# Performance work log

Measured on AMD Instinct MI355X. Metric: run time of the kernel, lower is better.

The kernel has to match this reference:

```python
import jax, jax.numpy as jnp
import numpy as np

B, N, D, NUM_CLASSES = 2048, 32768, 256, 100

def setup_inputs() -> dict:
    key = jax.random.key(0)
    k1, k2, k3 = jax.random.split(key, 3)
    x = jax.random.normal(k1, (B, D), dtype=jnp.float32)
    support_embeddings = jax.random.normal(k2, (N, D), dtype=jnp.float32)
    support_labels = jax.random.randint(k3, (N,), 0, NUM_CLASSES, dtype=jnp.int64)
    return {
        "x": x,
        "support_embeddings": support_embeddings,
        "support_labels": support_labels,
        "num_classes": NUM_CLASSES,
    }

def reference(x, support_embeddings, support_labels, num_classes):
    # Pairwise L2 distance [B, N] via ||q||^2 + ||s||^2 - 2 q.s (avoids [B,N,D] broadcast)
    q2 = jnp.sum(x * x, axis=1, keepdims=True)                 # [B, 1]
    s2 = jnp.sum(support_embeddings * support_embeddings, axis=1)  # [N]
    cross = jnp.einsum('bd,nd->bn', x, support_embeddings)     # [B, N]
    dist = jnp.sqrt(jnp.maximum(q2 + s2[None, :] - 2.0 * cross, 0.0))
    # topk(-dist, k=1) over support axis -> nearest neighbor index
    _, idx = jax.lax.top_k(-dist, 1)                           # [B, 1]
    idx = jnp.squeeze(idx, axis=1)                             # [B]
    labels = jnp.take(support_labels, idx, axis=0)             # [B]
    one_hot = jax.nn.one_hot(labels, num_classes, dtype=jnp.int32)  # [B, num_classes]
    return one_hot
```

## Files before the change

kernel.cpp:

```cpp
#include <hip/hip_runtime.h>

#define BQ 2048
#define NS 32768
#define DIM 256
#define NROWS (NS + BQ)

#define BMQ 128
#define BNS 128
#define BK 32
#define NST (DIM / BK)
#define GY (NS / BNS)
#define GX (BQ / BMQ)
#define EPS 0.08f
#define FBCH GY

typedef _Float16 f16;
typedef _Float16 f16x4 __attribute__((ext_vector_type(4)));
typedef _Float16 f16x8 __attribute__((ext_vector_type(8)));
typedef float    f32x4 __attribute__((ext_vector_type(4)));

__device__ __forceinline__ void gload16(const f16* g, f16* l) {
    __builtin_amdgcn_global_load_lds(
        (const __attribute__((address_space(1))) unsigned int*)g,
        (__attribute__((address_space(3))) unsigned int*)l, 16, 0, 0);
}

__device__ __forceinline__ const f16x8* fragp(const f16* base, int row, int q) {
    return (const f16x8*)(base + row * 32 + ((q ^ ((row >> 1) & 3)) << 3));
}

__global__ __launch_bounds__(256) void convert_kernel(
    const float* __restrict__ x, const float* __restrict__ sup,
    f16* __restrict__ xh, f16* __restrict__ sh,
    float* __restrict__ s2, int* __restrict__ fb_cnt) {
    if (blockIdx.x == 0 && threadIdx.x == 0) *fb_cnt = 0;
    const int wave = threadIdx.x >> 6, lane = threadIdx.x & 63;
    const int row = blockIdx.x * 4 + wave;
    if (row < NS) {
        float4 v = ((const float4*)(sup + (size_t)row * DIM))[lane];
        f16x4 hi;
        hi[0] = (f16)v.x; hi[1] = (f16)v.y; hi[2] = (f16)v.z; hi[3] = (f16)v.w;
        *(f16x4*)(sh + (size_t)row * DIM + lane * 4) = hi;
        float sum = v.x * v.x + v.y * v.y + v.z * v.z + v.w * v.w;
#pragma unroll
        for (int off = 32; off > 0; off >>= 1) sum += __shfl_xor(sum, off);
        if (lane == 0) s2[row] = sum;
    } else {
        const int q = row - NS;
        float4 v = ((const float4*)(x + (size_t)q * DIM))[lane];
        f16x4 hi;
        hi[0] = (f16)v.x; hi[1] = (f16)v.y; hi[2] = (f16)v.z; hi[3] = (f16)v.w;
        *(f16x4*)(xh + (size_t)q * DIM + lane * 4) = hi;
    }
}

__global__ __launch_bounds__(256) void knn_mfma(
    const f16* __restrict__ xh, const f16* __restrict__ sh,
    const float* __restrict__ s2g,
    float* __restrict__ pv1, float* __restrict__ pv2, int* __restrict__ pi1) {
    __shared__ f16 T[3][2][BMQ * 32];

    const int tid  = threadIdx.x;
    const int lane = tid & 63, wid = tid >> 6;
    const int l16  = lane & 15, quad = lane >> 4;

    const int id   = blockIdx.y * GX + blockIdx.x;
    const int xcd  = id & 7;
    const int slot = id >> 3;
    const int gx   = slot & (GX - 1);
    const int gy   = xcd * (GY / 8) + (slot >> 4);
    const int m0   = gx * BMQ;
    const int n0   = gy * BNS;

    const int rl = lane >> 2;
    const int qs = (lane & 3) ^ ((rl >> 1) & 3);
    const size_t srcoff = (size_t)rl * DIM + qs * 8;

    const f16* px0 = xh + (size_t)(m0 + wid * 32) * DIM + srcoff;
    const f16* px1 = px0 + (size_t)16 * DIM;
    const f16* ps0 = sh + (size_t)(n0 + wid * 32) * DIM + srcoff;
    const f16* ps1 = ps0 + (size_t)16 * DIM;
    const int dX = wid * 1024;

    f32x4 acc[2][8];
#pragma unroll
    for (int fi = 0; fi < 2; ++fi)
#pragma unroll
        for (int fj = 0; fj < 8; ++fj) acc[fi][fj] = (f32x4){0.f, 0.f, 0.f, 0.f};

    auto issue = [&](int s) {
        f16* bx = &T[s % 3][0][dX];
        f16* bs = &T[s % 3][1][dX];
        const int k0 = s * BK;
        gload16(px0 + k0, bx);
        gload16(px1 + k0, bx + 512);
        gload16(ps0 + k0, bs);
        gload16(ps1 + k0, bs + 512);
    };

    issue(0);
    issue(1);

#pragma unroll
    for (int s = 0; s < NST; ++s) {
        if (s < NST - 1)
            asm volatile("s_waitcnt vmcnt(4)\n\ts_barrier" ::: "memory");
        else
            asm volatile("s_waitcnt vmcnt(0)\n\ts_barrier" ::: "memory");
        if (s + 2 < NST) issue(s + 2);

        const f16* TX = &T[s % 3][0][0];
        const f16* TS = &T[s % 3][1][0];
        f16x8 A0 = *fragp(TX, wid * 32 + l16,      quad);
        f16x8 A1 = *fragp(TX, wid * 32 + 16 + l16, quad);
#pragma unroll
        for (int fj = 0; fj < 8; ++fj) {
            f16x8 B = *fragp(TS, fj * 16 + l16, quad);
            acc[0][fj] = __builtin_amdgcn_mfma_f32_16x16x32_f16(A0, B, acc[0][fj], 0, 0, 0);
            acc[1][fj] = __builtin_amdgcn_mfma_f32_16x16x32_f16(A1, B, acc[1][fj], 0, 0, 0);
        }
    }

    float s2v[8];
#pragma unroll
    for (int fj = 0; fj < 8; ++fj) s2v[fj] = s2g[n0 + fj * 16 + l16];
#pragma unroll
    for (int fi = 0; fi < 2; ++fi)
#pragma unroll
        for (int rg = 0; rg < 4; ++rg) {
            float bv1 = 3.4e38f, bv2 = 3.4e38f; int bi = 0;
#pragma unroll
            for (int fj = 0; fj < 8; ++fj) {
                float s = fmaf(-2.f, acc[fi][fj][rg], s2v[fj]);
                bv2 = fminf(bv2, fmaxf(bv1, s));
                bi  = (s < bv1) ? (n0 + fj * 16 + l16) : bi;
                bv1 = fminf(bv1, s);
            }
#pragma unroll
            for (int m = 1; m < 16; m <<= 1) {
                float ov1 = __shfl_xor(bv1, m);
                float ov2 = __shfl_xor(bv2, m);
                int   oi  = __shfl_xor(bi, m);
                float nb2 = fminf(fminf(bv2, ov2), fmaxf(bv1, ov1));
                bi  = (ov1 < bv1) ? oi : bi;
                bv1 = fminf(bv1, ov1);
                bv2 = nb2;
            }
            if (l16 == 0) {
                const int row = m0 + wid * 32 + fi * 16 + quad * 4 + rg;
                pv1[(size_t)row * GY + gy] = bv1;
                pv2[(size_t)row * GY + gy] = bv2;
                pi1[(size_t)row * GY + gy] = bi;
            }
        }
}

__global__ __launch_bounds__(128) void finalize2(
    const float* __restrict__ pv1, const float* __restrict__ pv2,
    const int* __restrict__ pi1, const int* __restrict__ labels,
    const int* __restrict__ ncp, int* __restrict__ out,
    int* __restrict__ fb_cnt, int* __restrict__ fb_list,
    float* __restrict__ qbest) {
    const int q = blockIdx.x, tid = threadIdx.x;
    __shared__ int s_label;
    if (tid < 64) {
        float bv1 = 3.4e38f, bv2 = 3.4e38f; int bi = 0;
        for (int t = tid; t < GY; t += 64) {
            float ov1 = pv1[(size_t)q * GY + t];
            float ov2 = pv2[(size_t)q * GY + t];
            int   oi  = pi1[(size_t)q * GY + t];
            float nb2 = fminf(fminf(bv2, ov2), fmaxf(bv1, ov1));
            bi  = (ov1 < bv1) ? oi : bi;
            bv1 = fminf(bv1, ov1);
            bv2 = nb2;
        }
#pragma unroll
        for (int m = 1; m < 64; m <<= 1) {
            float ov1 = __shfl_xor(bv1, m);
            float ov2 = __shfl_xor(bv2, m);
            int   oi  = __shfl_xor(bi, m);
            float nb2 = fminf(fminf(bv2, ov2), fmaxf(bv1, ov1));
            bi  = (ov1 < bv1) ? oi : bi;
            bv1 = fminf(bv1, ov1);
            bv2 = nb2;
        }
        if (tid == 0) {
            qbest[q] = bv1;
            if (bv2 - bv1 <= EPS) {
                int slot = atomicAdd(fb_cnt, 1);
                fb_list[slot] = q;
            }
            bool is64 = true;
            for (int i = 1; i < 128; i += 2)
                if (labels[i] != 0) { is64 = false; break; }
            s_label = is64 ? labels[2 * bi] : labels[bi];
        }
    }
    __syncthreads();
    const int nc = ncp[0], lbl = s_label;
    for (int c = tid; c < nc; c += 128)
        out[q * nc + c] = (c == lbl) ? 1 : 0;
}

__global__ __launch_bounds__(256) void fallback_scan(
    const float* __restrict__ x, const float* __restrict__ sup,
    const float* __restrict__ s2, const int* __restrict__ fb_cnt,
    const int* __restrict__ fb_list, const float* __restrict__ qbest,
    const float* __restrict__ pv1,
    float* __restrict__ fb_v, int* __restrict__ fb_i) {
    const int nslots = *fb_cnt;
    const int chunk = blockIdx.x;
    const int tid = threadIdx.x, lane = tid & 63, w = tid >> 6;
    __shared__ float wv[4];
    __shared__ int   wi[4];
    for (int slot = blockIdx.y; slot < nslots; slot += gridDim.y) {
        const int q = fb_list[slot];
        if (pv1[(size_t)q * GY + chunk] > qbest[q] + EPS) {
            if (tid == 0) {
                fb_v[(size_t)q * FBCH + chunk] = 3.4e38f;
                fb_i[(size_t)q * FBCH + chunk] = 0x7fffffff;
            }
            __syncthreads();
            continue;
        }
        const float4 xv = ((const float4*)(x + (size_t)q * DIM))[lane];
        float best = 3.4e38f; int bi = 0x7fffffff;
        const int base = chunk * BNS + w * 32;
#pragma unroll 4
        for (int r = 0; r < 32; ++r) {
            const int n = base + r;
            float4 sv = ((const float4*)(sup + (size_t)n * DIM))[lane];
            float d = fmaf(sv.x, xv.x,
                      fmaf(sv.y, xv.y,
                      fmaf(sv.z, xv.z, sv.w * xv.w)));
#pragma unroll
            for (int m = 32; m > 0; m >>= 1) d += __shfl_xor(d, m);
            float sc = s2[n] - 2.f * d;
            if (sc < best) { best = sc; bi = n; }
        }
        if (lane == 0) { wv[w] = best; wi[w] = bi; }
        __syncthreads();
        if (tid == 0) {
            float bv = wv[0]; int bx = wi[0];
#pragma unroll
            for (int t = 1; t < 4; ++t)
                if (wv[t] < bv || (wv[t] == bv && wi[t] < bx)) { bv = wv[t]; bx = wi[t]; }
            fb_v[(size_t)q * FBCH + chunk] = bv;
            fb_i[(size_t)q * FBCH + chunk] = bx;
        }
        __syncthreads();
    }
}

__global__ __launch_bounds__(64) void fallback_merge(
    const int* __restrict__ fb_cnt, const int* __restrict__ fb_list,
    const float* __restrict__ fb_v, const int* __restrict__ fb_i,
    const int* __restrict__ labels, const int* __restrict__ ncp,
    int* __restrict__ out) {
    const int nslots = *fb_cnt;
    const int lane = threadIdx.x;
    for (int slot = blockIdx.x; slot < nslots; slot += gridDim.x) {
        const int q = fb_list[slot];
        float v = 3.4e38f; int ix = 0x7fffffff;
        for (int t = lane; t < FBCH; t += 64) {
            float ov = fb_v[(size_t)q * FBCH + t];
            int   oi = fb_i[(size_t)q * FBCH + t];
            if (ov < v || (ov == v && oi < ix)) { v = ov; ix = oi; }
        }
#pragma unroll
        for (int m = 1; m < 64; m <<= 1) {
            float ov = __shfl_xor(v, m);
            int   oi = __shfl_xor(ix, m);
            if (ov < v || (ov == v && oi < ix)) { v = ov; ix = oi; }
        }
        bool is64 = true;
        for (int i = 1; i < 128; i += 2)
            if (labels[i] != 0) { is64 = false; break; }
        const int lbl = is64 ? labels[2 * ix] : labels[ix];
        const int nc = ncp[0];
        for (int c = lane; c < nc; c += 64)
            out[q * nc + c] = (c == lbl) ? 1 : 0;
    }
}

#define SBM 128
#define SBN 128
#define SBK 16
#define SNT 4
#define SGY (NS / (SBN * SNT))
#define SLDT (SBM + 4)

__global__ __launch_bounds__(256) void s2_kernel(const float* __restrict__ s,
                                                 float* __restrict__ s2) {
    int wave = threadIdx.x >> 6, lane = threadIdx.x & 63;
    int row = blockIdx.x * 4 + wave;
    const float4* p = (const float4*)(s + (size_t)row * DIM);
    float4 v = p[lane];
    float sum = v.x * v.x + v.y * v.y + v.z * v.z + v.w * v.w;
#pragma unroll
    for (int off = 32; off > 0; off >>= 1) sum += __shfl_xor(sum, off);
    if (lane == 0) s2[row] = sum;
}

__global__ __launch_bounds__(256) void knn_f32(const float* __restrict__ x,
                                               const float* __restrict__ sup,
                                               const float* __restrict__ s2g,
                                               float* __restrict__ pvals,
                                               int* __restrict__ pidx) {
    __shared__ float Xs[SBK][SLDT];
    __shared__ float Bs[SBK][SLDT];
    const int tid = threadIdx.x;
    const int tx = tid & 15, ty = tid >> 4;
    const int m0 = blockIdx.x * SBM, by = blockIdx.y;
    const int srow = tid >> 2, skq = (tid & 3) * 4;
    float rmin[8]; int ridx[8];
#pragma unroll
    for (int i = 0; i < 8; ++i) { rmin[i] = 3.4e38f; ridx[i] = 0x7fffffff; }
    const float* xr0 = x + (size_t)(m0 + srow) * DIM + skq;
    const float* xr1 = x + (size_t)(m0 + 64 + srow) * DIM + skq;
    for (int nt = 0; nt < SNT; ++nt) {
        const int n0 = (by * SNT + nt) * SBN;
        const float* sr0 = sup + (size_t)(n0 + srow) * DIM + skq;
        const float* sr1 = sup + (size_t)(n0 + 64 + srow) * DIM + skq;
        float acc[8][8];
#pragma unroll
        for (int i = 0; i < 8; ++i)
#pragma unroll
            for (int j = 0; j < 8; ++j) acc[i][j] = 0.0f;
        for (int kt = 0; kt < DIM / SBK; ++kt) {
            const int k0 = kt * SBK;
            float4 xv0 = *(const float4*)(xr0 + k0);
            float4 xv1 = *(const float4*)(xr1 + k0);
            float4 sv0 = *(const float4*)(sr0 + k0);
            float4 sv1 = *(const float4*)(sr1 + k0);
            __syncthreads();
            Xs[skq + 0][srow] = xv0.x; Xs[skq + 1][srow] = xv0.y;
            Xs[skq + 2][srow] = xv0.z; Xs[skq + 3][srow] = xv0.w;
            Xs[skq + 0][64 + srow] = xv1.x; Xs[skq + 1][64 + srow] = xv1.y;
            Xs[skq + 2][64 + srow] = xv1.z; Xs[skq + 3][64 + srow] = xv1.w;
            Bs[skq + 0][srow] = sv0.x; Bs[skq + 1][srow] = sv0.y;
            Bs[skq + 2][srow] = sv0.z; Bs[skq + 3][srow] = sv0.w;
            Bs[skq + 0][64 + srow] = sv1.x; Bs[skq + 1][64 + srow] = sv1.y;
            Bs[skq + 2][64 + srow] = sv1.z; Bs[skq + 3][64 + srow] = sv1.w;
            __syncthreads();
#pragma unroll
            for (int k = 0; k < SBK; ++k) {
                float4 a0 = *(const float4*)&Xs[k][ty * 4];
                float4 a1 = *(const float4*)&Xs[k][64 + ty * 4];
                float4 b0 = *(const float4*)&Bs[k][tx * 4];
                float4 b1 = *(const float4*)&Bs[k][64 + tx * 4];
                float a[8] = {a0.x, a0.y, a0.z, a0.w, a1.x, a1.y, a1.z, a1.w};
                float b[8] = {b0.x, b0.y, b0.z, b0.w, b1.x, b1.y, b1.z, b1.w};
#pragma unroll
                for (int i = 0; i < 8; ++i)
#pragma unroll
                    for (int j = 0; j < 8; ++j)
                        acc[i][j] = fmaf(a[i], b[j], acc[i][j]);
            }
        }
        const int nb0 = n0 + tx * 4, nb1 = n0 + 64 + tx * 4;
        float4 s20 = *(const float4*)(s2g + nb0);
        float4 s21 = *(const float4*)(s2g + nb1);
        float s2a[8] = {s20.x, s20.y, s20.z, s20.w, s21.x, s21.y, s21.z, s21.w};
        int nca[8] = {nb0, nb0 + 1, nb0 + 2, nb0 + 3, nb1, nb1 + 1, nb1 + 2, nb1 + 3};
#pragma unroll
        for (int i = 0; i < 8; ++i)
#pragma unroll
            for (int j = 0; j < 8; ++j) {
                float sc = fmaf(-2.0f, acc[i][j], s2a[j]);
                if (sc < rmin[i] || (sc == rmin[i] && nca[j] < ridx[i])) {
                    rmin[i] = sc; ridx[i] = nca[j];
                }
            }
    }
    __syncthreads();
    float* redv = (float*)Xs;
    int* redi = (int*)Bs;
#pragma unroll
    for (int i = 0; i < 8; ++i) {
        int mrow = (i < 4) ? (ty * 4 + i) : (64 + ty * 4 + (i - 4));
        redv[mrow * 16 + tx] = rmin[i];
        redi[mrow * 16 + tx] = ridx[i];
    }
    __syncthreads();
    if (tid < SBM) {
        float best = redv[tid * 16];
        int bi = redi[tid * 16];
#pragma unroll
        for (int t = 1; t < 16; ++t) {
            float v = redv[tid * 16 + t];
            int ix = redi[tid * 16 + t];
            if (v < best || (v == best && ix < bi)) { best = v; bi = ix; }
        }
        pvals[(size_t)(m0 + tid) * SGY + by] = best;
        pidx[(size_t)(m0 + tid) * SGY + by] = bi;
    }
}

__global__ __launch_bounds__(64) void finalize_f32(const float* __restrict__ pvals,
                                                   const int* __restrict__ pidx,
                                                   const int* __restrict__ labels,
                                                   const int* __restrict__ ncp,
                                                   int* __restrict__ out) {
    const int b = blockIdx.x, lane = threadIdx.x;
    float v = pvals[(size_t)b * SGY + lane];
    int ix = pidx[(size_t)b * SGY + lane];
#pragma unroll
    for (int off = 32; off > 0; off >>= 1) {
        float ov = __shfl_xor(v, off);
        int oi = __shfl_xor(ix, off);
        if (ov < v || (ov == v && oi < ix)) { v = ov; ix = oi; }
    }
    bool is64 = true;
    for (int i = 1; i < 128; i += 2)
        if (labels[i] != 0) { is64 = false; break; }
    const int lbl = is64 ? labels[2 * ix] : labels[ix];
    const int nc = ncp[0];
    for (int c = lane; c < nc; c += 64)
        out[b * nc + c] = (c == lbl) ? 1 : 0;
}

extern "C" void kernel_launch(void* const* d_in, const int* in_sizes, int n_in,
                              void* d_out, int out_size, void* d_ws, size_t ws_size,
                              hipStream_t stream) {
    const float* x      = (const float*)d_in[0];
    const float* sup    = (const float*)d_in[1];
    const int*   labels = (const int*)d_in[2];
    const int*   ncp    = (const int*)d_in[3];
    int* out = (int*)d_out;

    char* p = (char*)d_ws;
    float* s2      = (float*)p;           p += (size_t)NS * 4;
    float* pv1     = (float*)p;           p += (size_t)BQ * GY * 4;
    float* pv2     = (float*)p;           p += (size_t)BQ * GY * 4;
    int*   pi1     = (int*)p;             p += (size_t)BQ * GY * 4;
    int*   fb_cnt  = (int*)p;             p += 256;
    int*   fb_list = (int*)p;             p += (size_t)BQ * 4;
    float* qbest   = (float*)p;           p += (size_t)BQ * 4;
    float* fb_v    = (float*)p;           p += (size_t)BQ * FBCH * 4;
    int*   fb_i    = (int*)p;             p += (size_t)BQ * FBCH * 4;
    f16*   xh      = (f16*)p;             p += (size_t)BQ * DIM * 2;
    f16*   sh      = (f16*)p;             p += (size_t)NS * DIM * 2;
    const size_t need = (size_t)(p - (char*)d_ws);

    if (ws_size >= need) {
        convert_kernel<<<NROWS / 4, 256, 0, stream>>>(x, sup, xh, sh, s2, fb_cnt);
        dim3 grid(GX, GY);
        knn_mfma<<<grid, 256, 0, stream>>>(xh, sh, s2, pv1, pv2, pi1);
        finalize2<<<BQ, 128, 0, stream>>>(pv1, pv2, pi1, labels, ncp, out,
                                          fb_cnt, fb_list, qbest);
        dim3 fbgrid(FBCH, 64);
        fallback_scan<<<fbgrid, 256, 0, stream>>>(x, sup, s2, fb_cnt, fb_list,
                                                  qbest, pv1, fb_v, fb_i);
        fallback_merge<<<64, 64, 0, stream>>>(fb_cnt, fb_list, fb_v, fb_i, labels, ncp, out);
    } else {
        float* ss2   = (float*)d_ws;
        float* pvals = ss2 + NS;
        int*   pidx  = (int*)(pvals + (size_t)BQ * SGY);
        s2_kernel<<<NS / 4, 256, 0, stream>>>(sup, ss2);
        dim3 sgrid(BQ / SBM, SGY);
        knn_f32<<<sgrid, 256, 0, stream>>>(x, sup, ss2, pvals, pidx);
        finalize_f32<<<BQ, 64, 0, stream>>>(pvals, pidx, labels, ncp, out);
    }
}
```

Before: 157.4 us.

## Load query fragments directly to registers and widen K-step to 64

The query (A) tile no longer goes through LDS. Each wave loads its A fragments straight from global memory into registers and prefetches the next K-step one iteration ahead. Only the support (B) tile is staged in LDS, with a new XOR swizzle for 64-wide rows, and the K-step doubles to halve the number of barrier iterations. The vmcnt waits are adjusted to count the extra register loads, and launch bounds now request 3 blocks per CU. This trades LDS traffic and barriers for more VGPR pressure and uncoalesced per-lane global loads of the query rows.

```diff
diff --git a/kernel.cpp b/kernel.cpp
--- a/kernel.cpp
+++ b/kernel.cpp
@@ -7,7 +7,7 @@
 
 #define BMQ 128
 #define BNS 128
-#define BK 32
+#define BK 64
 #define NST (DIM / BK)
 #define GY (NS / BNS)
 #define GX (BQ / BMQ)
@@ -19,14 +19,16 @@
 typedef _Float16 f16x8 __attribute__((ext_vector_type(8)));
 typedef float    f32x4 __attribute__((ext_vector_type(4)));
 
+#define MEMFENCE asm volatile("" ::: "memory")
+
 __device__ __forceinline__ void gload16(const f16* g, f16* l) {
     __builtin_amdgcn_global_load_lds(
         (const __attribute__((address_space(1))) unsigned int*)g,
         (__attribute__((address_space(3))) unsigned int*)l, 16, 0, 0);
 }
 
-__device__ __forceinline__ const f16x8* fragp(const f16* base, int row, int q) {
-    return (const f16x8*)(base + row * 32 + ((q ^ ((row >> 1) & 3)) << 3));
+__device__ __forceinline__ const f16x8* fragB(const f16* base, int row, int cell) {
+    return (const f16x8*)(base + row * 64 + ((cell ^ (row & 7)) << 3));
 }
 
 __global__ __launch_bounds__(256) void convert_kernel(
@@ -54,11 +56,11 @@
     }
 }
 
-__global__ __launch_bounds__(256) void knn_mfma(
+__global__ __launch_bounds__(256, 3) void knn_mfma(
     const f16* __restrict__ xh, const f16* __restrict__ sh,
     const float* __restrict__ s2g,
     float* __restrict__ pv1, float* __restrict__ pv2, int* __restrict__ pi1) {
-    __shared__ f16 T[3][2][BMQ * 32];
+    __shared__ f16 T[3][BNS * BK];
 
     const int tid  = threadIdx.x;
     const int lane = tid & 63, wid = tid >> 6;
@@ -72,15 +74,12 @@
     const int m0   = gx * BMQ;
     const int n0   = gy * BNS;
 
-    const int rl = lane >> 2;
-    const int qs = (lane & 3) ^ ((rl >> 1) & 3);
-    const size_t srcoff = (size_t)rl * DIM + qs * 8;
-
-    const f16* px0 = xh + (size_t)(m0 + wid * 32) * DIM + srcoff;
-    const f16* px1 = px0 + (size_t)16 * DIM;
-    const f16* ps0 = sh + (size_t)(n0 + wid * 32) * DIM + srcoff;
-    const f16* ps1 = ps0 + (size_t)16 * DIM;
-    const int dX = wid * 1024;
+    const int rl8 = lane >> 3;
+    const int cl  = lane & 7;
+    const f16* psrc = sh + (size_t)(n0 + wid * 32 + rl8) * DIM + ((cl ^ rl8) << 3);
+    const int dS = wid * 2048;
+
+    const f16* pA = xh + (size_t)(m0 + wid * 32 + l16) * DIM + quad * 8;
 
     f32x4 acc[2][8];
 #pragma unroll
@@ -88,37 +87,54 @@
 #pragma unroll
         for (int fj = 0; fj < 8; ++fj) acc[fi][fj] = (f32x4){0.f, 0.f, 0.f, 0.f};
 
-    auto issue = [&](int s) {
-        f16* bx = &T[s % 3][0][dX];
-        f16* bs = &T[s % 3][1][dX];
-        const int k0 = s * BK;
-        gload16(px0 + k0, bx);
-        gload16(px1 + k0, bx + 512);
-        gload16(ps0 + k0, bs);
-        gload16(ps1 + k0, bs + 512);
+    auto issueS = [&](int s) {
+        f16* bs = &T[s % 3][dS];
+        const f16* src = psrc + (size_t)s * BK;
+        gload16(src,            bs);
+        gload16(src +  8 * DIM, bs + 512);
+        gload16(src + 16 * DIM, bs + 1024);
+        gload16(src + 24 * DIM, bs + 1536);
     };
 
-    issue(0);
-    issue(1);
+    issueS(0);
+    issueS(1);
+    MEMFENCE;
+    f16x8 A0c = *(const f16x8*)(pA);
+    f16x8 A1c = *(const f16x8*)(pA + 32);
+    f16x8 A2c = *(const f16x8*)(pA + 16 * DIM);
+    f16x8 A3c = *(const f16x8*)(pA + 16 * DIM + 32);
 
 #pragma unroll
     for (int s = 0; s < NST; ++s) {
+        MEMFENCE;
+        f16x8 A0n, A1n, A2n, A3n;
+        if (s + 1 < NST) {
+            const f16* pn = pA + (s + 1) * BK;
+            A0n = *(const f16x8*)(pn);
+            A1n = *(const f16x8*)(pn + 32);
+            A2n = *(const f16x8*)(pn + 16 * DIM);
+            A3n = *(const f16x8*)(pn + 16 * DIM + 32);
+        }
         if (s < NST - 1)
+            asm volatile("s_waitcnt vmcnt(12)\n\ts_barrier" ::: "memory");
+        else
             asm volatile("s_waitcnt vmcnt(4)\n\ts_barrier" ::: "memory");
-        else
-            asm volatile("s_waitcnt vmcnt(0)\n\ts_barrier" ::: "memory");
-        if (s + 2 < NST) issue(s + 2);
-
-        const f16* TX = &T[s % 3][0][0];
-        const f16* TS = &T[s % 3][1][0];
-        f16x8 A0 = *fragp(TX, wid * 32 + l16,      quad);
-        f16x8 A1 = *fragp(TX, wid * 32 + 16 + l16, quad);
+        if (s + 2 < NST) issueS(s + 2);
+
+        const f16* TS = &T[s % 3][0];
 #pragma unroll
         for (int fj = 0; fj < 8; ++fj) {
-            f16x8 B = *fragp(TS, fj * 16 + l16, quad);
-            acc[0][fj] = __builtin_amdgcn_mfma_f32_16x16x32_f16(A0, B, acc[0][fj], 0, 0, 0);
-            acc[1][fj] = __builtin_amdgcn_mfma_f32_16x16x32_f16(A1, B, acc[1][fj], 0, 0, 0);
-        }
+            f16x8 B0 = *fragB(TS, fj * 16 + l16, quad);
+            acc[0][fj] = __builtin_amdgcn_mfma_f32_16x16x32_f16(A0c, B0, acc[0][fj], 0, 0, 0);
+            acc[1][fj] = __builtin_amdgcn_mfma_f32_16x16x32_f16(A2c, B0, acc[1][fj], 0, 0, 0);
+        }
+#pragma unroll
+        for (int fj = 0; fj < 8; ++fj) {
+            f16x8 B1 = *fragB(TS, fj * 16 + l16, 4 + quad);
+            acc[0][fj] = __builtin_amdgcn_mfma_f32_16x16x32_f16(A1c, B1, acc[0][fj], 0, 0, 0);
+            acc[1][fj] = __builtin_amdgcn_mfma_f32_16x16x32_f16(A3c, B1, acc[1][fj], 0, 0, 0);
+        }
+        A0c = A0n; A1c = A1n; A2c = A2n; A3c = A3n;
     }
 
     float s2v[8];
```

New measurement: 163.1 us. 3.7% more time.

## Load query fragments directly to registers and stage whole support tile in LDS

Applied to the files above, without the earlier changes.

Query A-fragments now go straight from global memory into registers for the full K depth, bypassing LDS. The support tile's full 256-wide slab is loaded into LDS in one shot. This replaces the 3-stage pipeline with a single wait and barrier, and adds a min-blocks-per-CU hint of 2. It removes per-stage barriers and LDS traffic for the query operand, but increases register use and gives up overlap between loads and MFMA within a block.

```diff
diff --git a/kernel.cpp b/kernel.cpp
--- a/kernel.cpp
+++ b/kernel.cpp
@@ -8,7 +8,7 @@
 #define BMQ 128
 #define BNS 128
 #define BK 32
-#define NST (DIM / BK)
+#define NPL (DIM / BK)
 #define GY (NS / BNS)
 #define GX (BQ / BMQ)
 #define EPS 0.08f
@@ -54,11 +54,11 @@
     }
 }
 
-__global__ __launch_bounds__(256) void knn_mfma(
+__global__ __launch_bounds__(256, 2) void knn_mfma(
     const f16* __restrict__ xh, const f16* __restrict__ sh,
     const float* __restrict__ s2g,
     float* __restrict__ pv1, float* __restrict__ pv2, int* __restrict__ pi1) {
-    __shared__ f16 T[3][2][BMQ * 32];
+    __shared__ f16 T[NPL][BNS * 32];
 
     const int tid  = threadIdx.x;
     const int lane = tid & 63, wid = tid >> 6;
@@ -75,12 +75,24 @@
     const int rl = lane >> 2;
     const int qs = (lane & 3) ^ ((rl >> 1) & 3);
     const size_t srcoff = (size_t)rl * DIM + qs * 8;
-
-    const f16* px0 = xh + (size_t)(m0 + wid * 32) * DIM + srcoff;
-    const f16* px1 = px0 + (size_t)16 * DIM;
     const f16* ps0 = sh + (size_t)(n0 + wid * 32) * DIM + srcoff;
     const f16* ps1 = ps0 + (size_t)16 * DIM;
-    const int dX = wid * 1024;
+    const int dS = wid * 1024;
+
+    const f16* pA = xh + (size_t)(m0 + wid * 32 + l16) * DIM + quad * 8;
+
+#pragma unroll
+    for (int s = 0; s < NPL; ++s) {
+        f16* bs = &T[s][dS];
+        gload16(ps0 + s * BK, bs);
+        gload16(ps1 + s * BK, bs + 512);
+    }
+    f16x8 A[2][NPL];
+#pragma unroll
+    for (int s = 0; s < NPL; ++s) {
+        A[0][s] = *(const f16x8*)(pA + s * BK);
+        A[1][s] = *(const f16x8*)(pA + 16 * DIM + s * BK);
+    }
 
     f32x4 acc[2][8];
 #pragma unroll
@@ -88,36 +100,16 @@
 #pragma unroll
         for (int fj = 0; fj < 8; ++fj) acc[fi][fj] = (f32x4){0.f, 0.f, 0.f, 0.f};
 
-    auto issue = [&](int s) {
-        f16* bx = &T[s % 3][0][dX];
-        f16* bs = &T[s % 3][1][dX];
-        const int k0 = s * BK;
-        gload16(px0 + k0, bx);
-        gload16(px1 + k0, bx + 512);
-        gload16(ps0 + k0, bs);
-        gload16(ps1 + k0, bs + 512);
-    };
-
-    issue(0);
-    issue(1);
-
-#pragma unroll
-    for (int s = 0; s < NST; ++s) {
-        if (s < NST - 1)
-            asm volatile("s_waitcnt vmcnt(4)\n\ts_barrier" ::: "memory");
-        else
-            asm volatile("s_waitcnt vmcnt(0)\n\ts_barrier" ::: "memory");
-        if (s + 2 < NST) issue(s + 2);
-
-        const f16* TX = &T[s % 3][0][0];
-        const f16* TS = &T[s % 3][1][0];
-        f16x8 A0 = *fragp(TX, wid * 32 + l16,      quad);
-        f16x8 A1 = *fragp(TX, wid * 32 + 16 + l16, quad);
+    asm volatile("s_waitcnt vmcnt(0)\n\ts_barrier" ::: "memory");
+
+#pragma unroll
+    for (int s = 0; s < NPL; ++s) {
+        const f16* TS = &T[s][0];
 #pragma unroll
         for (int fj = 0; fj < 8; ++fj) {
             f16x8 B = *fragp(TS, fj * 16 + l16, quad);
-            acc[0][fj] = __builtin_amdgcn_mfma_f32_16x16x32_f16(A0, B, acc[0][fj], 0, 0, 0);
-            acc[1][fj] = __builtin_amdgcn_mfma_f32_16x16x32_f16(A1, B, acc[1][fj], 0, 0, 0);
+            acc[0][fj] = __builtin_amdgcn_mfma_f32_16x16x32_f16(A[0][s], B, acc[0][fj], 0, 0, 0);
+            acc[1][fj] = __builtin_amdgcn_mfma_f32_16x16x32_f16(A[1][s], B, acc[1][fj], 0, 0, 0);
         }
     }
 
```

Result: slower. 173.9 us (+10.5%).
